# Kernel optimization log

Hardware: AMD Instinct MI355X
Metric: run time of the kernel (lower is better)

Reference implementation:

```python
import jax, jax.numpy as jnp
import numpy as np

W, H = 256, 256          # image width (x) and height (y); image indexed [x, y] like the torch code
N = 8192                 # depth-sorted visible gaussians
TILE = 16                # tile_size default
CHUNK = 128              # gaussians composited per scan step (N % CHUNK == 0)
MIN_WEIGHT = 1e-6        # early-termination threshold from render_pixel


def setup_inputs() -> dict:
    key = jax.random.key(0)
    k1, k2, k3, k4, k5 = jax.random.split(key, 5)
    # pixel-space means, uniformly over the image
    points_xy = jax.random.uniform(k1, (N, 2), dtype=jnp.float32) * jnp.array([W, H], jnp.float32)
    # SPD inverse 2D covariances: Sigma = R diag(var) R^T, inv = R diag(1/var) R^T
    theta = jax.random.uniform(k2, (N,), dtype=jnp.float32) * (2.0 * np.pi)
    sig = jax.random.uniform(k3, (N, 2), dtype=jnp.float32, minval=1.5, maxval=8.0)
    var = sig ** 2
    ct, st = jnp.cos(theta), jnp.sin(theta)
    R = jnp.stack([jnp.stack([ct, -st], -1), jnp.stack([st, ct], -1)], -2)  # [N,2,2]
    inverse_covariance = jnp.einsum('nij,nj,nkj->nik', R, 1.0 / var, R)
    # radius = ceil(2.5 * sqrt(max eigenvalue)) as in compute_radius
    radius = jnp.ceil(2.5 * jnp.sqrt(jnp.max(var, axis=1)))
    colors = jax.random.uniform(k4, (N, 3), dtype=jnp.float32)
    opacity = jax.random.normal(k5, (N,), dtype=jnp.float32)  # pre-sigmoid logits
    return dict(points_xy=points_xy, inverse_covariance=inverse_covariance,
                radius=radius, colors=colors, opacity=opacity)


def _rasterize(points_xy, inverse_covariance, radius, colors, opacity):
    px = jnp.arange(W, dtype=jnp.float32)[:, None]   # [W,1] pixel x coords
    py = jnp.arange(H, dtype=jnp.float32)[None, :]   # [1,H] pixel y coords
    # tile origin for each pixel (tile-based culling as in render_image)
    tile_x0 = ((jnp.arange(W) // TILE) * TILE).astype(jnp.float32)[:, None]  # [W,1]
    tile_y0 = ((jnp.arange(H) // TILE) * TILE).astype(jnp.float32)[None, :]  # [1,H]
    # per-gaussian bounding boxes (preprocess)
    min_x = jnp.floor(points_xy[:, 0] - radius); max_x = jnp.ceil(points_xy[:, 0] + radius)
    min_y = jnp.floor(points_xy[:, 1] - radius); max_y = jnp.ceil(points_xy[:, 1] + radius)

    n_chunks = N // CHUNK
    def chunk(a):
        return a.reshape((n_chunks, CHUNK) + a.shape[1:])
    xs = dict(mx=chunk(points_xy[:, 0]), my=chunk(points_xy[:, 1]),
              a=chunk(inverse_covariance[:, 0, 0]), b=chunk(inverse_covariance[:, 0, 1]),
              c=chunk(inverse_covariance[:, 1, 1]),
              mnx=chunk(min_x), mxx=chunk(max_x), mny=chunk(min_y), mxy=chunk(max_y),
              col=chunk(colors), op=chunk(opacity))

    @jax.checkpoint
    def body(carry, ch):
        T, color = carry  # T: [W,H] remaining transmittance; color: [W,H,3]
        dx = px[None] - ch['mx'][:, None, None]  # [C,W,1]
        dy = py[None] - ch['my'][:, None, None]  # [C,1,H]
        # mahalanobis form d^T Sigma^{-1} d with symmetric inv cov [[a,b],[b,c]]
        q = (ch['a'][:, None, None] * dx * dx
             + 2.0 * ch['b'][:, None, None] * dx * dy
             + ch['c'][:, None, None] * dy * dy)              # [C,W,H]
        alpha = jnp.exp(-0.5 * q) * jax.nn.sigmoid(ch['op'])[:, None, None]
        # gaussian participates for a pixel iff its bbox intersects that pixel's tile
        in_tile = ((ch['mnx'][:, None, None] <= tile_x0[None] + TILE)
                   & (ch['mxx'][:, None, None] >= tile_x0[None])
                   & (ch['mny'][:, None, None] <= tile_y0[None] + TILE)
                   & (ch['mxy'][:, None, None] >= tile_y0[None]))   # [C,W,H]
        alpha = jnp.where(in_tile, alpha, 0.0)
        cum = jnp.cumprod(1.0 - alpha, axis=0)                 # inclusive prefix of (1-alpha)
        T_before = T[None] * jnp.concatenate([jnp.ones_like(cum[:1]), cum[:-1]], axis=0)
        # original: test_weight = T_before*(1-alpha); terminate (skip contribution) if < min_weight
        include = (T[None] * cum) >= MIN_WEIGHT
        contrib = jnp.where(include, T_before * alpha, 0.0)   # [C,W,H]
        color = color + jnp.einsum('cwh,cd->whd', contrib, ch['col'])
        return (T * cum[-1], color), None

    init = (jnp.ones((W, H), jnp.float32), jnp.zeros((W, H, 3), jnp.float32))
    (_, color), _ = jax.lax.scan(body, init, xs)
    return color  # [W,H,3] image indexed [x,y]


def reference(points_xy, inverse_covariance, radius, colors, opacity):
    return _rasterize(points_xy, inverse_covariance, radius, colors, opacity)
```

## Files before the change

### kernel.cpp

```cpp
#include <hip/hip_runtime.h>
#include <hip/hip_fp16.h>

#define WIDTH   256
#define HEIGHT  256
#define NG      8192
#define TILE_SZ 16
#define MINW    1e-6f
#define BLK     1024
#define NBATCH  (NG / BLK)
#define NWAVE   (BLK / 64)
#define NSEG    16
#define PXB     128
#define RSZ     512
#define KC      (-0.72134752044f)

__global__ __launch_bounds__(BLK, 8) void raster_kernel(
    const float* __restrict__ pts,
    const float* __restrict__ icov,
    const float* __restrict__ rad,
    const float* __restrict__ cols,
    const float* __restrict__ opac,
    float* __restrict__ out)
{
    __shared__ unsigned long long s_ball[NBATCH * NWAVE];
    __shared__ int s_pfx[NBATCH * NWAVE];
    __shared__ __align__(16) char s_pool[32768];
    unsigned short* s_list = (unsigned short*)s_pool;
    float4* s_g = (float4*)(s_pool + 16384);
    float*  s_red = (float*)s_pool;
    __shared__ float s_P[NSEG][PXB];

    const int tid  = threadIdx.x;
    const int lane = tid & 63;
    const int wave = tid >> 6;
    const int seg  = wave;
    const float tx0 = (float)(blockIdx.x * TILE_SZ);
    const float ty0 = (float)(blockIdx.y * TILE_SZ);
    const float tx1 = tx0 + (float)TILE_SZ;
    const float ty1 = ty0 + (float)TILE_SZ;

    unsigned int hitbits = 0;
    #pragma unroll
    for (int b = 0; b < NBATCH; ++b) {
        const int g = b * BLK + tid;
        const float2 p = ((const float2*)pts)[g];
        const float  r = rad[g];
        bool hit = (floorf(p.x - r) <= tx1) & (ceilf(p.x + r) >= tx0)
                 & (floorf(p.y - r) <= ty1) & (ceilf(p.y + r) >= ty0);
        unsigned long long m = __ballot(hit);
        if (lane == 0) s_ball[b * NWAVE + wave] = m;
        if (hit) hitbits |= (1u << b);
    }
    __syncthreads();
    if (wave == 0) {
        int v0 = __popcll(s_ball[lane]);
        int v1 = __popcll(s_ball[64 + lane]);
        #pragma unroll
        for (int d = 1; d < 64; d <<= 1) {
            const int t0 = __shfl_up(v0, d);
            const int t1 = __shfl_up(v1, d);
            if (lane >= d) { v0 += t0; v1 += t1; }
        }
        s_pfx[lane] = v0;
        s_pfx[64 + lane] = v1 + __shfl(v0, 63);
    }
    __syncthreads();
    const int count = s_pfx[127];
    {
        unsigned int hb = hitbits;
        const unsigned long long ltmask = (1ull << lane) - 1ull;
        while (hb) {
            const int b = __ffs(hb) - 1;  hb &= hb - 1;
            const int idx = b * NWAVE + wave;
            const unsigned long long m = s_ball[idx];
            const int bs = idx ? s_pfx[idx - 1] : 0;
            s_list[bs + __popcll(m & ltmask)] = (unsigned short)(b * BLK + tid);
        }
    }
    __syncthreads();

    const int pr = tid & 63;
    const int xl = pr >> 3, yp = pr & 7;
    const float fx  = tx0 + (float)(blockIdx.z * 8 + xl);
    const float fyA = ty0 + (float)(2 * yp);
    const int pA = xl * 16 + 2 * yp;
    const int pxi[2] = {pA, pA + 1};
    float Tpx = 1.0f;
    float acc[3][2];
    #pragma unroll
    for (int c = 0; c < 3; ++c) { acc[c][0] = 0.0f; acc[c][1] = 0.0f; }

    for (int base = 0; base < count; base += RSZ) {
        const int n = min(RSZ, count - base);
        if (tid < n) {
            const int g = s_list[base + tid];
            const float2 p = ((const float2*)pts)[g];
            const float4 ic = ((const float4*)icov)[g];
            const float op = 1.0f / (1.0f + __expf(-opac[g]));
            const __half2 h = __floats2half2_rn(cols[3 * g], cols[3 * g + 1]);
            unsigned rgbits; __builtin_memcpy(&rgbits, &h, 4);
            s_g[tid * 2 + 0] = make_float4(p.x, p.y, KC * ic.x, 2.0f * KC * ic.y);
            s_g[tid * 2 + 1] = make_float4(KC * ic.w, op, __uint_as_float(rgbits),
                                           cols[3 * g + 2]);
        }
        __syncthreads();

        const int L  = (n + NSEG - 1) >> 4;
        const int i0 = seg * L;
        const int i1 = min(i0 + L, n);

        float P[2] = {1.f, 1.f};
        float l[3][2];
        #pragma unroll
        for (int c = 0; c < 3; ++c) { l[c][0] = 0.0f; l[c][1] = 0.0f; }

        #pragma unroll 2
        for (int i = i0; i < i1; ++i) {
            const float4 g0 = s_g[i * 2 + 0];
            const float4 g1 = s_g[i * 2 + 1];
            const float dx  = fx - g0.x;
            const float axx = (g0.z * dx) * dx;
            const float bdx = g0.w * dx;
            const float dyA = fyA - g0.y, dyB = dyA + 1.0f;
            const float qv[2] = { fmaf(dyA, fmaf(g1.x, dyA, bdx), axx),
                                  fmaf(dyB, fmaf(g1.x, dyB, bdx), axx) };
            const unsigned rgbits = __float_as_uint(g1.z);
            __half2 h; __builtin_memcpy(&h, &rgbits, 4);
            const float2 rg = __half22float2(h);
            #pragma unroll
            for (int k = 0; k < 2; ++k) {
                const float a = g1.y * __builtin_amdgcn_exp2f(qv[k]);
                const float w = P[k] * a;
                l[0][k] = fmaf(w, rg.x, l[0][k]);
                l[1][k] = fmaf(w, rg.y, l[1][k]);
                l[2][k] = fmaf(w, g1.w, l[2][k]);
                P[k] = fmaf(-a, P[k], P[k]);
            }
        }
        s_P[seg][pxi[0]] = P[0];
        s_P[seg][pxi[1]] = P[1];
        __syncthreads();

        if (tid < PXB) {
            float run = Tpx;
            #pragma unroll
            for (int s = 0; s < NSEG; ++s) {
                const float Pv = s_P[s][tid];
                s_P[s][tid] = run;
                run *= Pv;
            }
            Tpx = run;
        }
        __syncthreads();

        float Tin[2];
        bool gated[2]; bool anyg = false;
        #pragma unroll
        for (int k = 0; k < 2; ++k) {
            Tin[k] = s_P[seg][pxi[k]];
            const bool alive = (Tin[k] >= MINW);
            gated[k] = alive && (Tin[k] * P[k] < MINW);
            if (alive && !gated[k]) {
                acc[0][k] = fmaf(Tin[k], l[0][k], acc[0][k]);
                acc[1][k] = fmaf(Tin[k], l[1][k], acc[1][k]);
                acc[2][k] = fmaf(Tin[k], l[2][k], acc[2][k]);
            }
            anyg |= gated[k];
        }
        if (__ballot(anyg) != 0ull) {
            float Tl[2] = {Tin[0], Tin[1]};
            for (int i = i0; i < i1; ++i) {
                const float4 g0 = s_g[i * 2 + 0];
                const float4 g1 = s_g[i * 2 + 1];
                const float dx  = fx - g0.x;
                const float axx = (g0.z * dx) * dx;
                const float bdx = g0.w * dx;
                const float dyA = fyA - g0.y, dyB = dyA + 1.0f;
                const float qv[2] = { fmaf(dyA, fmaf(g1.x, dyA, bdx), axx),
                                      fmaf(dyB, fmaf(g1.x, dyB, bdx), axx) };
                const unsigned rgbits = __float_as_uint(g1.z);
                __half2 h; __builtin_memcpy(&h, &rgbits, 4);
                const float2 rg = __half22float2(h);
                #pragma unroll
                for (int k = 0; k < 2; ++k) {
                    const float a  = g1.y * __builtin_amdgcn_exp2f(qv[k]);
                    const float Tn = Tl[k] * (1.0f - a);
                    const float w  = (gated[k] && Tn >= MINW) ? Tl[k] * a : 0.0f;
                    acc[0][k] = fmaf(w, rg.x, acc[0][k]);
                    acc[1][k] = fmaf(w, rg.y, acc[1][k]);
                    acc[2][k] = fmaf(w, g1.w, acc[2][k]);
                    Tl[k] = Tn;
                }
            }
        }
        const bool mydead = (tid < PXB) ? (Tpx < MINW) : true;
        if (__syncthreads_count(mydead) == BLK) break;
    }

    #pragma unroll
    for (int k = 0; k < 2; ++k) {
        s_red[(seg * PXB + pxi[k]) * 3 + 0] = acc[0][k];
        s_red[(seg * PXB + pxi[k]) * 3 + 1] = acc[1][k];
        s_red[(seg * PXB + pxi[k]) * 3 + 2] = acc[2][k];
    }
    __syncthreads();
    if (tid < PXB * 3) {
        const int p  = tid / 3;
        const int ch = tid - 3 * p;
        float v = 0.0f;
        #pragma unroll
        for (int s = 0; s < NSEG; ++s) v += s_red[(s * PXB + p) * 3 + ch];
        const int x = blockIdx.x * TILE_SZ + blockIdx.z * 8 + (p >> 4);
        const int y = blockIdx.y * TILE_SZ + (p & 15);
        out[(x * HEIGHT + y) * 3 + ch] = v;
    }
}

extern "C" void kernel_launch(void* const* d_in, const int* in_sizes, int n_in,
                              void* d_out, int out_size, void* d_ws, size_t ws_size,
                              hipStream_t stream) {
    const float* pts  = (const float*)d_in[0];
    const float* icov = (const float*)d_in[1];
    const float* rad  = (const float*)d_in[2];
    const float* cols = (const float*)d_in[3];
    const float* opac = (const float*)d_in[4];
    float* out = (float*)d_out;
    dim3 grid(WIDTH / TILE_SZ, HEIGHT / TILE_SZ, 2);
    raster_kernel<<<grid, dim3(BLK), 0, stream>>>(pts, icov, rad, cols, opac, out);
}
```

Baseline: 78.12 us.

## Process full 16x16 tile per block with four pixels per thread

Each block now covers the whole 16x16 tile instead of half of it, so the grid drops its z dimension. Each thread composites four vertically adjacent pixels instead of two, reusing each loaded gaussian record across more pixels. Per-tile culling, list building and the gaussian staging pass now run once per tile instead of twice. In exchange the grid has half as many blocks, register pressure and shared memory grow, and launch bounds fall to 4 blocks, all of which lower occupancy and parallelism.

```diff
diff --git a/kernel.cpp b/kernel.cpp
--- a/kernel.cpp
+++ b/kernel.cpp
@@ -10,11 +10,11 @@
 #define NBATCH  (NG / BLK)
 #define NWAVE   (BLK / 64)
 #define NSEG    16
-#define PXB     128
+#define PXB     256
 #define RSZ     512
 #define KC      (-0.72134752044f)
 
-__global__ __launch_bounds__(BLK, 8) void raster_kernel(
+__global__ __launch_bounds__(BLK, 4) void raster_kernel(
     const float* __restrict__ pts,
     const float* __restrict__ icov,
     const float* __restrict__ rad,
@@ -24,11 +24,12 @@
 {
     __shared__ unsigned long long s_ball[NBATCH * NWAVE];
     __shared__ int s_pfx[NBATCH * NWAVE];
-    __shared__ __align__(16) char s_pool[32768];
+    __shared__ __align__(16) char s_pool[49152];
     unsigned short* s_list = (unsigned short*)s_pool;
     float4* s_g = (float4*)(s_pool + 16384);
     float*  s_red = (float*)s_pool;
-    __shared__ float s_P[NSEG][PXB];
+    __shared__ float4 s_P4[NSEG][64];
+    float* s_Pf = (float*)s_P4;
 
     const int tid  = threadIdx.x;
     const int lane = tid & 63;
@@ -79,16 +80,17 @@
     }
     __syncthreads();
 
-    const int pr = tid & 63;
-    const int xl = pr >> 3, yp = pr & 7;
-    const float fx  = tx0 + (float)(blockIdx.z * 8 + xl);
-    const float fyA = ty0 + (float)(2 * yp);
-    const int pA = xl * 16 + 2 * yp;
-    const int pxi[2] = {pA, pA + 1};
+    const int xl = lane >> 2;
+    const int yb = lane & 3;
+    const float fx  = tx0 + (float)xl;
+    const float fy0 = ty0 + (float)(4 * yb);
+    const int pA = xl * 16 + 4 * yb;
     float Tpx = 1.0f;
-    float acc[3][2];
+    float acc[3][4];
     #pragma unroll
-    for (int c = 0; c < 3; ++c) { acc[c][0] = 0.0f; acc[c][1] = 0.0f; }
+    for (int c = 0; c < 3; ++c)
+        #pragma unroll
+        for (int k = 0; k < 4; ++k) acc[c][k] = 0.0f;
 
     for (int base = 0; base < count; base += RSZ) {
         const int n = min(RSZ, count - base);
@@ -109,10 +111,12 @@
         const int i0 = seg * L;
         const int i1 = min(i0 + L, n);
 
-        float P[2] = {1.f, 1.f};
-        float l[3][2];
-        #pragma unroll
-        for (int c = 0; c < 3; ++c) { l[c][0] = 0.0f; l[c][1] = 0.0f; }
+        float P[4] = {1.f, 1.f, 1.f, 1.f};
+        float l[3][4];
+        #pragma unroll
+        for (int c = 0; c < 3; ++c)
+            #pragma unroll
+            for (int k = 0; k < 4; ++k) l[c][k] = 0.0f;
 
         #pragma unroll 2
         for (int i = i0; i < i1; ++i) {
@@ -121,15 +125,15 @@
             const float dx  = fx - g0.x;
             const float axx = (g0.z * dx) * dx;
             const float bdx = g0.w * dx;
-            const float dyA = fyA - g0.y, dyB = dyA + 1.0f;
-            const float qv[2] = { fmaf(dyA, fmaf(g1.x, dyA, bdx), axx),
-                                  fmaf(dyB, fmaf(g1.x, dyB, bdx), axx) };
+            const float dy0 = fy0 - g0.y;
             const unsigned rgbits = __float_as_uint(g1.z);
             __half2 h; __builtin_memcpy(&h, &rgbits, 4);
             const float2 rg = __half22float2(h);
             #pragma unroll
-            for (int k = 0; k < 2; ++k) {
-                const float a = g1.y * __builtin_amdgcn_exp2f(qv[k]);
+            for (int k = 0; k < 4; ++k) {
+                const float dyk = dy0 + (float)k;
+                const float q = fmaf(dyk, fmaf(g1.x, dyk, bdx), axx);
+                const float a = g1.y * __builtin_amdgcn_exp2f(q);
                 const float w = P[k] * a;
                 l[0][k] = fmaf(w, rg.x, l[0][k]);
                 l[1][k] = fmaf(w, rg.y, l[1][k]);
@@ -137,27 +141,26 @@
                 P[k] = fmaf(-a, P[k], P[k]);
             }
         }
-        s_P[seg][pxi[0]] = P[0];
-        s_P[seg][pxi[1]] = P[1];
+        s_P4[seg][lane] = make_float4(P[0], P[1], P[2], P[3]);
         __syncthreads();
 
         if (tid < PXB) {
             float run = Tpx;
             #pragma unroll
             for (int s = 0; s < NSEG; ++s) {
-                const float Pv = s_P[s][tid];
-                s_P[s][tid] = run;
+                const float Pv = s_Pf[s * PXB + tid];
+                s_Pf[s * PXB + tid] = run;
                 run *= Pv;
             }
             Tpx = run;
         }
         __syncthreads();
 
-        float Tin[2];
-        bool gated[2]; bool anyg = false;
-        #pragma unroll
-        for (int k = 0; k < 2; ++k) {
-            Tin[k] = s_P[seg][pxi[k]];
+        const float4 Tv = s_P4[seg][lane];
+        const float Tin[4] = {Tv.x, Tv.y, Tv.z, Tv.w};
+        bool gated[4]; bool anyg = false;
+        #pragma unroll
+        for (int k = 0; k < 4; ++k) {
             const bool alive = (Tin[k] >= MINW);
             gated[k] = alive && (Tin[k] * P[k] < MINW);
             if (alive && !gated[k]) {
@@ -168,22 +171,22 @@
             anyg |= gated[k];
         }
         if (__ballot(anyg) != 0ull) {
-            float Tl[2] = {Tin[0], Tin[1]};
+            float Tl[4] = {Tin[0], Tin[1], Tin[2], Tin[3]};
             for (int i = i0; i < i1; ++i) {
                 const float4 g0 = s_g[i * 2 + 0];
                 const float4 g1 = s_g[i * 2 + 1];
                 const float dx  = fx - g0.x;
                 const float axx = (g0.z * dx) * dx;
                 const float bdx = g0.w * dx;
-                const float dyA = fyA - g0.y, dyB = dyA + 1.0f;
-                const float qv[2] = { fmaf(dyA, fmaf(g1.x, dyA, bdx), axx),
-                                      fmaf(dyB, fmaf(g1.x, dyB, bdx), axx) };
+                const float dy0 = fy0 - g0.y;
                 const unsigned rgbits = __float_as_uint(g1.z);
                 __half2 h; __builtin_memcpy(&h, &rgbits, 4);
                 const float2 rg = __half22float2(h);
                 #pragma unroll
-                for (int k = 0; k < 2; ++k) {
-                    const float a  = g1.y * __builtin_amdgcn_exp2f(qv[k]);
+                for (int k = 0; k < 4; ++k) {
+                    const float dyk = dy0 + (float)k;
+                    const float q = fmaf(dyk, fmaf(g1.x, dyk, bdx), axx);
+                    const float a  = g1.y * __builtin_amdgcn_exp2f(q);
                     const float Tn = Tl[k] * (1.0f - a);
                     const float w  = (gated[k] && Tn >= MINW) ? Tl[k] * a : 0.0f;
                     acc[0][k] = fmaf(w, rg.x, acc[0][k]);
@@ -197,11 +200,11 @@
         if (__syncthreads_count(mydead) == BLK) break;
     }
 
-    #pragma unroll
-    for (int k = 0; k < 2; ++k) {
-        s_red[(seg * PXB + pxi[k]) * 3 + 0] = acc[0][k];
-        s_red[(seg * PXB + pxi[k]) * 3 + 1] = acc[1][k];
-        s_red[(seg * PXB + pxi[k]) * 3 + 2] = acc[2][k];
+    {
+        float4* dst = (float4*)&s_red[(seg * PXB + pA) * 3];
+        dst[0] = make_float4(acc[0][0], acc[1][0], acc[2][0], acc[0][1]);
+        dst[1] = make_float4(acc[1][1], acc[2][1], acc[0][2], acc[1][2]);
+        dst[2] = make_float4(acc[2][2], acc[0][3], acc[1][3], acc[2][3]);
     }
     __syncthreads();
     if (tid < PXB * 3) {
@@ -210,7 +213,7 @@
         float v = 0.0f;
         #pragma unroll
         for (int s = 0; s < NSEG; ++s) v += s_red[(s * PXB + p) * 3 + ch];
-        const int x = blockIdx.x * TILE_SZ + blockIdx.z * 8 + (p >> 4);
+        const int x = blockIdx.x * TILE_SZ + (p >> 4);
         const int y = blockIdx.y * TILE_SZ + (p & 15);
         out[(x * HEIGHT + y) * 3 + ch] = v;
     }
@@ -225,6 +228,6 @@
     const float* cols = (const float*)d_in[3];
     const float* opac = (const float*)d_in[4];
     float* out = (float*)d_out;
-    dim3 grid(WIDTH / TILE_SZ, HEIGHT / TILE_SZ, 2);
+    dim3 grid(WIDTH / TILE_SZ, HEIGHT / TILE_SZ, 1);
     raster_kernel<<<grid, dim3(BLK), 0, stream>>>(pts, icov, rad, cols, opac, out);
 }
```

Result: no change. 78.74 us (+0.8%).
